# Optimization experiments

Hardware: AMD Instinct MI355X
Metric: run time of the kernel (lower is better)

The kernel has to match this reference:

```python
import jax, jax.numpy as jnp
import numpy as np

NUM_HEADS = 8
DIM = 256
HEAD_DIM = DIM // NUM_HEADS  # 32
CPB_HIDDEN = 512
FFN_HIDDEN = 1024


def _relative_position_cpb(query_size, key_size, pretrain_size):
    # TransNeXt-style continuous position bias table + index (query==key grid here)
    qh, qw = query_size
    kh, kw = key_size
    ph, pw = pretrain_size
    aqh = np.arange(qh, dtype=np.float64)
    akh = np.arange(kh, dtype=np.float64)
    aqw = np.arange(qw, dtype=np.float64)
    akw = np.arange(kw, dtype=np.float64)
    kH, kW = np.meshgrid(akh, akw, indexing='ij')
    qH, qW = np.meshgrid(aqh, aqw, indexing='ij')
    rel_h = (qH.reshape(-1)[:, None] - kH.reshape(-1)[None, :]) / (ph - 1) * 8.0
    rel_w = (qW.reshape(-1)[:, None] - kW.reshape(-1)[None, :]) / (pw - 1) * 8.0
    rel = np.stack([rel_h, rel_w], axis=-1).reshape(-1, 2)
    table, idx = np.unique(rel, return_inverse=True, axis=0)
    table = np.sign(table) * np.log2(np.abs(table) + 1.0) / np.log2(8.0)
    return idx.astype(np.int32).reshape(-1), table.astype(np.float32)


def setup_inputs() -> dict:
    key = jax.random.key(0)
    ks = jax.random.split(key, 16)
    B, C, H, W = 8, 256, 128, 128
    q = jax.random.normal(ks[0], (B, C, H, W), dtype=jnp.float32)
    kv = jax.random.normal(ks[1], (B, C, H, W), dtype=jnp.float32)
    rel_idx_np, rel_table_np = _relative_position_cpb((32, 32), (32, 32), (32, 32))
    s = 0.02
    inp = {
        'q': q,
        'kv': kv,
        'rel_pos_index': jnp.asarray(rel_idx_np),
        'rel_coords_table': jnp.asarray(rel_table_np),
        'Wq': jax.random.normal(ks[2], (DIM, DIM), jnp.float32) * s,
        'bq': jnp.zeros((DIM,), jnp.float32),
        'Wkv': jax.random.normal(ks[3], (DIM, 2 * DIM), jnp.float32) * s,
        'bkv': jnp.zeros((2 * DIM,), jnp.float32),
        'Wo': jax.random.normal(ks[4], (DIM, DIM), jnp.float32) * s,
        'bo': jnp.zeros((DIM,), jnp.float32),
        'cpb_w1': jax.random.normal(ks[5], (2, CPB_HIDDEN), jnp.float32) * s,
        'cpb_b1': jnp.zeros((CPB_HIDDEN,), jnp.float32),
        'cpb_w2': jax.random.normal(ks[6], (CPB_HIDDEN, NUM_HEADS), jnp.float32) * s,
        'cpb_b2': jnp.zeros((NUM_HEADS,), jnp.float32),
        'ffn_w1': jax.random.normal(ks[7], (DIM, FFN_HIDDEN), jnp.float32) * s,
        'ffn_b1': jnp.zeros((FFN_HIDDEN,), jnp.float32),
        'ffn_w2': jax.random.normal(ks[8], (FFN_HIDDEN, DIM), jnp.float32) * s,
        'ffn_b2': jnp.zeros((DIM,), jnp.float32),
        'ln_g': jnp.ones((DIM,), jnp.float32),
        'ln_b': jnp.zeros((DIM,), jnp.float32),
    }
    return inp


def _resize_bilinear(x, size):
    # matches torch F.interpolate(mode='bilinear', align_corners=False)
    return jax.image.resize(x, (x.shape[0], x.shape[1], size[0], size[1]),
                            method='linear', antialias=False)


def _layernorm(x, g, b, eps=1e-5):
    mu = jnp.mean(x, axis=-1, keepdims=True)
    var = jnp.mean(jnp.square(x - mu), axis=-1, keepdims=True)
    return (x - mu) * jax.lax.rsqrt(var + eps) * g + b


def _fpn_forward(q, kv, rel_pos_index, rel_coords_table, Wq, bq, Wkv, bkv, Wo, bo,
                 cpb_w1, cpb_b1, cpb_w2, cpb_b2, ffn_w1, ffn_b1, ffn_w2, ffn_b2, ln_g, ln_b):
    x = q
    B, C, H, W = q.shape
    pH = H // 4
    pW = H // 4  # note: original code uses h for both, matching square inputs
    N = pH * pW

    qd = jax.nn.relu(_resize_bilinear(q, (pH, pW)))   # [B,C,pH,pW] (dropout p=0)
    kvd = jax.nn.relu(_resize_bilinear(kv, (pH, pW)))
    qt = qd.reshape(B, C, N).transpose(0, 2, 1)   # [B,N,C]
    kvt = kvd.reshape(B, C, N).transpose(0, 2, 1)  # [B,N,C]

    # --- BVAM: cross-attention with continuous relative position bias ---
    qh = (qt @ Wq + bq).reshape(B, N, NUM_HEADS, HEAD_DIM).transpose(0, 2, 1, 3)  # [B,h,N,d]
    kvp = (kvt @ Wkv + bkv).reshape(B, N, 2, NUM_HEADS, HEAD_DIM).transpose(2, 0, 3, 1, 4)
    k, v = kvp[0], kvp[1]  # [B,h,N,d]

    cpb = jax.nn.relu(rel_coords_table @ cpb_w1 + cpb_b1) @ cpb_w2 + cpb_b2  # [L,h]
    bias = cpb[rel_pos_index].reshape(N, N, NUM_HEADS).transpose(2, 0, 1)    # [h,N,N]

    scale = 1.0 / jnp.sqrt(jnp.float32(HEAD_DIM))
    logits = jnp.einsum('bhnd,bhmd->bhnm', qh, k) * scale + bias[None]
    attn = jax.nn.softmax(logits, axis=-1)
    out = jnp.einsum('bhnm,bhmd->bhnd', attn, v)
    out = out.transpose(0, 2, 1, 3).reshape(B, N, C) @ Wo + bo  # [B,N,C]

    # --- FFN (post-norm, gelu) ---
    ff = jax.nn.gelu(out @ ffn_w1 + ffn_b1, approximate=False) @ ffn_w2 + ffn_b2
    y = _layernorm(out + ff, ln_g, ln_b)  # [B,N,C]

    # back to spatial, upsample, residual
    y = y.transpose(0, 2, 1).reshape(B, C, pH, pW)
    y = jax.nn.relu(_resize_bilinear(y, (H, W)))
    return x + y


def reference(q, kv, rel_pos_index, rel_coords_table, Wq, bq, Wkv, bkv, Wo, bo,
              cpb_w1, cpb_b1, cpb_w2, cpb_b2, ffn_w1, ffn_b1, ffn_w2, ffn_b2, ln_g, ln_b):
    return _fpn_forward(q, kv, rel_pos_index, rel_coords_table, Wq, bq, Wkv, bkv, Wo, bo,
                        cpb_w1, cpb_b1, cpb_w2, cpb_b2, ffn_w1, ffn_b1, ffn_w2, ffn_b2, ln_g, ln_b)
```

## Files before the change

### kernel.cpp

```cpp
#include <hip/hip_runtime.h>
#include <hip/hip_bf16.h>
#include <hip/hip_fp16.h>

typedef __hip_bfloat16 bf16;
typedef __attribute__((ext_vector_type(8))) __bf16 bf16x8;
typedef __attribute__((ext_vector_type(4))) __bf16 bf16x4;
typedef __attribute__((ext_vector_type(4))) float f32x4;
typedef __attribute__((ext_vector_type(4))) float f4;

__device__ __forceinline__ void gload_lds16(const bf16* g, bf16* l)
{
    __builtin_amdgcn_global_load_lds((const __attribute__((address_space(1))) void*)g,
                                     (__attribute__((address_space(3))) void*)l, 16, 0, 0);
}

__global__ __launch_bounds__(256) void prep_kernel(
    const float* __restrict__ tab, const float* __restrict__ w1, const float* __restrict__ b1,
    const float* __restrict__ w2, const float* __restrict__ b2, float* __restrict__ cpbout, int L, int ncpb,
    const float* __restrict__ Wq, const float* __restrict__ Wkv, const float* __restrict__ Wo,
    const float* __restrict__ fw1, const float* __restrict__ fw2,
    bf16* __restrict__ WqT, bf16* __restrict__ WkvT, bf16* __restrict__ WoT,
    bf16* __restrict__ W1T, bf16* __restrict__ W2T,
    const float* __restrict__ qsrc, const float* __restrict__ kvsrc,
    bf16* __restrict__ qdst, bf16* __restrict__ kvdst)
{
    __shared__ float o[32][33];
    const int t = threadIdx.x;
    int bid = blockIdx.x;
    if (bid < ncpb) {
        int l = bid * 32 + (t >> 3);
        int js = t & 7;
        bool valid = l < L;
        float t0 = valid ? tab[2 * l] : 0.f, t1 = valid ? tab[2 * l + 1] : 0.f;
        float acc[8];
#pragma unroll
        for (int hh = 0; hh < 8; ++hh) acc[hh] = 0.f;
        for (int j = js; j < 512; j += 8) {
            float hv = fmaxf(t0 * w1[j] + t1 * w1[512 + j] + b1[j], 0.f);
            f4 w2a = *(const f4*)&w2[j * 8];
            f4 w2b = *(const f4*)&w2[j * 8 + 4];
#pragma unroll
            for (int hh = 0; hh < 4; ++hh) { acc[hh] += hv * w2a[hh]; acc[4 + hh] += hv * w2b[hh]; }
        }
#pragma unroll
        for (int d = 1; d < 8; d <<= 1)
#pragma unroll
            for (int hh = 0; hh < 8; ++hh) acc[hh] += __shfl_xor(acc[hh], d);
        if (js == 0 && valid)
#pragma unroll
            for (int hh = 0; hh < 8; ++hh) cpbout[(size_t)hh * L + l] = acc[hh] + b2[hh];
        return;
    }
    bid -= ncpb;
    if (bid < 768) {
        const float* W; bf16* WT; int K, N, base;
        if (bid < 64)        { W = Wq;  WT = WqT;  K = 256;  N = 256;  base = 0; }
        else if (bid < 192)  { W = Wkv; WT = WkvT; K = 256;  N = 512;  base = 64; }
        else if (bid < 256)  { W = Wo;  WT = WoT;  K = 256;  N = 256;  base = 192; }
        else if (bid < 512)  { W = fw1; WT = W1T;  K = 256;  N = 1024; base = 256; }
        else                 { W = fw2; WT = W2T;  K = 1024; N = 256;  base = 512; }
        int lid = bid - base;
        int tn = N >> 5;
        int k0 = (lid / tn) << 5, n0 = (lid % tn) << 5;
        {
            int r = t >> 3, cc = (t & 7) * 4;
            *(f4*)&o[r][cc] = *(const f4*)&W[(size_t)(k0 + r) * N + n0 + cc];
        }
        __syncthreads();
        {
            int n = t >> 3, kk = (t & 7) * 4;
            bf16 tmp[4];
#pragma unroll
            for (int i = 0; i < 4; ++i) tmp[i] = (bf16)o[kk + i][n];
            *(bf16x4*)&WT[(size_t)(n0 + n) * K + k0 + kk] = *(const bf16x4*)tmp;
        }
        return;
    }
    bid -= 768;
    {
        const float* src = bid < 2048 ? qsrc : kvsrc;
        bf16* dst = bid < 2048 ? qdst : kvdst;
        int bb2 = bid & 2047;
        int cc = bb2 & 7, i = (bb2 >> 3) & 31, b = bb2 >> 8;
#pragma unroll
        for (int p = 0; p < 4; ++p) {
            int id = p * 256 + t;
            int c = id >> 5, j = id & 31;
            const float* r = src + ((size_t)(b * 256 + cc * 32 + c) * 128 + 4 * i + 1) * 128 + 4 * j;
            float4 r1 = *(const float4*)r;
            float4 r2 = *(const float4*)(r + 128);
            o[c][j] = 0.25f * (r1.y + r1.z + r2.y + r2.z);
        }
        __syncthreads();
        {
            int j = t >> 3, c4 = (t & 7) * 4;
            bf16 tmp[4];
#pragma unroll
            for (int k = 0; k < 4; ++k) tmp[k] = (bf16)fmaxf(o[c4 + k][j], 0.f);
            *(bf16x4*)&dst[(size_t)(b * 1024 + i * 32 + j) * 256 + cc * 32 + c4] = *(const bf16x4*)tmp;
        }
    }
}

template<int BM, int BN>
__device__ __forceinline__ void gemm_core(
    const bf16* __restrict__ A, const bf16* __restrict__ BT, int K,
    int m0, int n0, bf16* As, bf16* Bs, f32x4 (&acc)[BM / 32][BN / 32])
{
    constexpr int MI = BM / 32, NJ = BN / 32;
    const int tid = threadIdx.x;
    const int lane = tid & 63, wid = tid >> 6;
    const int lo = lane & 15, hi = lane >> 4;
    const int wr = wid >> 1, wc = wid & 1;
#pragma unroll
    for (int i = 0; i < MI; ++i)
#pragma unroll
        for (int j = 0; j < NJ; ++j) acc[i][j] = f32x4{0.f, 0.f, 0.f, 0.f};

    for (int k0 = 0; k0 < K; k0 += 64) {
        __syncthreads();
#pragma unroll
        for (int p = 0; p < BM / 32; ++p) {
            int f = p * 256 + wid * 64 + lane;
            int row = f >> 3, cs = f & 7;
            gload_lds16(&A[(size_t)(m0 + row) * K + k0 + ((cs ^ (row & 7)) * 8)],
                        As + (size_t)(p * 256 + wid * 64) * 8);
        }
#pragma unroll
        for (int p = 0; p < BN / 32; ++p) {
            int f = p * 256 + wid * 64 + lane;
            int row = f >> 3, cs = f & 7;
            gload_lds16(&BT[(size_t)(n0 + row) * K + k0 + ((cs ^ (row & 7)) * 8)],
                        Bs + (size_t)(p * 256 + wid * 64) * 8);
        }
        __syncthreads();
        bf16x8 af[2][MI], bfr[2][NJ];
#pragma unroll
        for (int kk = 0; kk < 2; ++kk) {
#pragma unroll
            for (int i = 0; i < MI; ++i) {
                int row = wr * (BM / 2) + i * 16 + lo;
                af[kk][i] = *(const bf16x8*)&As[row * 64 + (((kk * 4 + hi) ^ (lo & 7)) * 8)];
            }
#pragma unroll
            for (int j = 0; j < NJ; ++j) {
                int row = wc * (BN / 2) + j * 16 + lo;
                bfr[kk][j] = *(const bf16x8*)&Bs[row * 64 + (((kk * 4 + hi) ^ (lo & 7)) * 8)];
            }
        }
#pragma unroll
        for (int kk = 0; kk < 2; ++kk)
#pragma unroll
            for (int i = 0; i < MI; ++i)
#pragma unroll
                for (int j = 0; j < NJ; ++j)
                    acc[i][j] = __builtin_amdgcn_mfma_f32_16x16x32_bf16(af[kk][i], bfr[kk][j], acc[i][j], 0, 0, 0);
    }
}

template<int BM, int BN>
__global__ __launch_bounds__(256) void gemm_bt(
    const bf16* __restrict__ A, const bf16* __restrict__ BT,
    const float* __restrict__ bias, bf16* __restrict__ Cb, float* __restrict__ Cf,
    const bf16* __restrict__ resid, int M, int N, int K, int act)
{
    constexpr int MI = BM / 32, NJ = BN / 32;
    __shared__ __align__(16) bf16 As[BM * 64];
    __shared__ __align__(16) bf16 Bs[BN * 64];
    const int tid = threadIdx.x;
    const int lane = tid & 63, wid = tid >> 6;
    const int lo = lane & 15, hi = lane >> 4;
    const int m0 = blockIdx.x * BM, n0 = blockIdx.y * BN;
    const int wr = wid >> 1, wc = wid & 1;
    f32x4 acc[MI][NJ];
    gemm_core<BM, BN>(A, BT, K, m0, n0, As, Bs, acc);
#pragma unroll
    for (int i = 0; i < MI; ++i)
#pragma unroll
        for (int j = 0; j < NJ; ++j) {
            int col = n0 + wc * (BN / 2) + j * 16 + lo;
            float bv = bias[col];
#pragma unroll
            for (int r = 0; r < 4; ++r) {
                int row = m0 + wr * (BM / 2) + i * 16 + hi * 4 + r;
                float v = acc[i][j][r] + bv;
                if (act == 1) v = 0.5f * v * (1.f + erff(v * 0.70710678118654752f));
                if (resid) v += (float)resid[(size_t)row * N + col];
                if (Cb) Cb[(size_t)row * N + col] = (bf16)v;
                else    Cf[(size_t)row * N + col] = v;
            }
        }
}

__global__ __launch_bounds__(256) void gemm_qkv(
    const bf16* __restrict__ qt, const bf16* __restrict__ WqT, const float* __restrict__ bq,
    bf16* __restrict__ qhb,
    const bf16* __restrict__ kvt, const bf16* __restrict__ WkvT, const float* __restrict__ bkv,
    bf16* __restrict__ kvpb, bf16* __restrict__ vT,
    const int* __restrict__ ridx, const float* __restrict__ cpbh,
    bf16* __restrict__ biasF, int L)
{
    __shared__ __align__(16) bf16 As[64 * 64];
    __shared__ __align__(16) bf16 Bs[64 * 64];
    const int tid = threadIdx.x;
    const int lane = tid & 63, wid = tid >> 6;
    const int lo = lane & 15, hi = lane >> 4;
    const int by = blockIdx.y;
    if (by >= 12) {
        __shared__ int rix[32][32];
        int id = (by - 12) * 128 + blockIdx.x;
        int qtb = id >> 5, mt = id & 31;
        {
            int q = tid >> 3, m4 = (tid & 7) * 4;
            *(int4*)&rix[q][m4] = *(const int4*)&ridx[(size_t)(qtb * 32 + q) * 1024 + mt * 32 + m4];
        }
        __syncthreads();
        const int qj = (tid >> 6) & 1, hg = tid >> 7;
        int lidx[8];
#pragma unroll
        for (int j = 0; j < 8; ++j) {
            int kf = j >> 2, r = j & 3;
            lidx[j] = rix[qj * 16 + lo][kf * 16 + hi * 4 + r];
        }
#pragma unroll
        for (int hh = 0; hh < 4; ++hh) {
            int h = hg * 4 + hh;
            const float* ct = cpbh + (size_t)h * L;
            bf16 vals[8];
#pragma unroll
            for (int j = 0; j < 8; ++j) vals[j] = (bf16)ct[lidx[j]];
            size_t off = ((((size_t)(h * 32 + qtb) * 32 + mt) * 2 + qj) * 64 + lane) * 8;
            *(bf16x8*)&biasF[off] = *(const bf16x8*)vals;
        }
        return;
    }
    const int wr = wid >> 1, wc = wid & 1;
    const bf16 *A, *BT; const float* bias; int n0;
    if (by < 4)      { A = qt;  BT = WqT;  bias = bq;  n0 = by * 64; }
    else             { A = kvt; BT = WkvT; bias = bkv; n0 = (by - 4) * 64; }
    const int m0 = blockIdx.x * 64;
    f32x4 acc[2][2];
    gemm_core<64, 64>(A, BT, 256, m0, n0, As, Bs, acc);
#pragma unroll
    for (int i = 0; i < 2; ++i)
#pragma unroll
        for (int j = 0; j < 2; ++j) {
            int col = n0 + wc * 32 + j * 16 + lo;
            float bv = bias[col];
            if (by < 4) {
#pragma unroll
                for (int r = 0; r < 4; ++r) {
                    int row = m0 + wr * 32 + i * 16 + hi * 4 + r;
                    qhb[(size_t)row * 256 + col] = (bf16)(acc[i][j][r] + bv);
                }
            } else if (by < 8) {
#pragma unroll
                for (int r = 0; r < 4; ++r) {
                    int row = m0 + wr * 32 + i * 16 + hi * 4 + r;
                    kvpb[(size_t)row * 512 + col] = (bf16)(acc[i][j][r] + bv);
                }
            } else {
                int vcol = col - 256;
                int h = vcol >> 5, d = vcol & 31;
                int b = m0 >> 10;
                int mbase = (m0 & 1023) + wr * 32 + i * 16 + hi * 4;
                bf16 tmp[4];
#pragma unroll
                for (int r = 0; r < 4; ++r) tmp[r] = (bf16)(acc[i][j][r] + bv);
                *(bf16x4*)&vT[(size_t)((b * 8 + h) * 32 + d) * 1024 + mbase] = *(const bf16x4*)tmp;
            }
        }
}

__global__ __launch_bounds__(256) void ffn2_ln_kernel(
    const bf16* __restrict__ A, const bf16* __restrict__ BT,
    const float* __restrict__ bias, const bf16* __restrict__ resid,
    const float* __restrict__ g, const float* __restrict__ bb,
    bf16* __restrict__ ysp)
{
    __shared__ __align__(16) bf16 As[16 * 64];
    __shared__ __align__(16) bf16 Bs[256 * 64];
    __shared__ float buf[16][260];
    const int tid = threadIdx.x;
    const int lane = tid & 63, wid = tid >> 6;
    const int lo = lane & 15, hi = lane >> 4;
    const int m0 = blockIdx.x * 16;
    f32x4 acc[4];
#pragma unroll
    for (int j = 0; j < 4; ++j) acc[j] = f32x4{0.f, 0.f, 0.f, 0.f};

    for (int k0 = 0; k0 < 1024; k0 += 64) {
        __syncthreads();
        if (tid < 128) {
            int row = tid >> 3, cs = tid & 7;
            gload_lds16(&A[(size_t)(m0 + row) * 1024 + k0 + ((cs ^ (row & 7)) * 8)],
                        As + (size_t)(wid * 64) * 8);
        }
#pragma unroll
        for (int p = 0; p < 8; ++p) {
            int f = p * 256 + tid, row = f >> 3, cs = f & 7;
            gload_lds16(&BT[(size_t)row * 1024 + k0 + ((cs ^ (row & 7)) * 8)],
                        Bs + (size_t)(p * 256 + wid * 64) * 8);
        }
        __syncthreads();
        bf16x8 af[2], bfr[2][4];
#pragma unroll
        for (int kk = 0; kk < 2; ++kk) {
            af[kk] = *(const bf16x8*)&As[lo * 64 + (((kk * 4 + hi) ^ (lo & 7)) * 8)];
#pragma unroll
            for (int j = 0; j < 4; ++j) {
                int row = wid * 64 + j * 16 + lo;
                bfr[kk][j] = *(const bf16x8*)&Bs[row * 64 + (((kk * 4 + hi) ^ (lo & 7)) * 8)];
            }
        }
#pragma unroll
        for (int kk = 0; kk < 2; ++kk)
#pragma unroll
            for (int j = 0; j < 4; ++j)
                acc[j] = __builtin_amdgcn_mfma_f32_16x16x32_bf16(af[kk], bfr[kk][j], acc[j], 0, 0, 0);
    }
#pragma unroll
    for (int j = 0; j < 4; ++j) {
        int col = wid * 64 + j * 16 + lo;
        float bv = bias[col];
#pragma unroll
        for (int r = 0; r < 4; ++r) {
            int lr = hi * 4 + r;
            buf[lr][col] = acc[j][r] + bv + (float)resid[(size_t)(m0 + lr) * 256 + col];
        }
    }
    __syncthreads();
#pragma unroll
    for (int rr = 0; rr < 4; ++rr) {
        int row = wid * 4 + rr;
        f4 x = *(const f4*)&buf[row][lane * 4];
        float s = x[0] + x[1] + x[2] + x[3];
#pragma unroll
        for (int d = 1; d < 64; d <<= 1) s += __shfl_xor(s, d);
        float mean = s * (1.f / 256.f);
        f4 dv = {x[0] - mean, x[1] - mean, x[2] - mean, x[3] - mean};
        float s2 = dv[0] * dv[0] + dv[1] * dv[1] + dv[2] * dv[2] + dv[3] * dv[3];
#pragma unroll
        for (int d = 1; d < 64; d <<= 1) s2 += __shfl_xor(s2, d);
        float rstd = rsqrtf(s2 * (1.f / 256.f) + 1e-5f);
        f4 o = {dv[0] * rstd, dv[1] * rstd, dv[2] * rstd, dv[3] * rstd};
        *(f4*)&buf[row][lane * 4] = o;
    }
    __syncthreads();
    float gc = g[tid], bc = bb[tid];
    int b = m0 >> 10, n0l = m0 & 1023;
    bf16* dst = &ysp[((size_t)(b * 256 + tid) << 10) + n0l];
#pragma unroll
    for (int p = 0; p < 2; ++p) {
        bf16 tmp[8];
#pragma unroll
        for (int k = 0; k < 8; ++k) tmp[k] = (bf16)(buf[p * 8 + k][tid] * gc + bc);
        *(bf16x8*)&dst[p * 8] = *(const bf16x8*)tmp;
    }
}

__global__ __launch_bounds__(256) void attn_kernel(
    const bf16* __restrict__ qh, const bf16* __restrict__ kvp, const bf16* __restrict__ vT,
    const bf16* __restrict__ biasF, bf16* __restrict__ attnout)
{
    __shared__ __align__(16) bf16 Ps[4][32 * 40];
    __shared__ __align__(16) __half accs[4][32][34];
    __shared__ float pm[4][32], pl[4][32];
    const int tid = threadIdx.x, lane = tid & 63, wid = tid >> 6;
    const int lo = lane & 15, hi = lane >> 4;
    const int qt = blockIdx.x, n0 = qt * 32;
    const int h = blockIdx.y;
    const int b = blockIdx.z;
    const float scale = 0.17677669529663687f;
    const f32x4 zero4 = {0.f, 0.f, 0.f, 0.f};

    bf16x8 qf[2];
#pragma unroll
    for (int qj = 0; qj < 2; ++qj)
        qf[qj] = *(const bf16x8*)&qh[(size_t)(b * 1024 + n0 + qj * 16 + lo) * 256 + h * 32 + hi * 8];

    f32x4 acc[2][2];
#pragma unroll
    for (int i = 0; i < 2; ++i)
#pragma unroll
        for (int j = 0; j < 2; ++j) acc[i][j] = zero4;
    float mrow[2] = {-1e30f, -1e30f}, lrow[2] = {0.f, 0.f};

    bf16* Pw = Ps[wid];

    for (int t = wid; t < 32; t += 4) {
        const int m0 = t * 32;
        bf16x8 kfr0 = *(const bf16x8*)&kvp[(size_t)(b * 1024 + m0 + lo) * 512 + h * 32 + hi * 8];
        bf16x8 kfr1 = *(const bf16x8*)&kvp[(size_t)(b * 1024 + m0 + 16 + lo) * 512 + h * 32 + hi * 8];
        bf16x8 va0 = *(const bf16x8*)&vT[(size_t)((b * 8 + h) * 32 + lo) * 1024 + m0 + hi * 8];
        bf16x8 va1 = *(const bf16x8*)&vT[(size_t)((b * 8 + h) * 32 + 16 + lo) * 1024 + m0 + hi * 8];
        size_t boff = (((size_t)(h * 32 + qt) * 32 + t) * 2 * 64 + lane) * 8;
        bf16x8 bv0 = *(const bf16x8*)&biasF[boff];
        bf16x8 bv1 = *(const bf16x8*)&biasF[boff + 512];

        f32x4 s[2][2];
        s[0][0] = __builtin_amdgcn_mfma_f32_16x16x32_bf16(kfr0, qf[0], zero4, 0, 0, 0);
        s[0][1] = __builtin_amdgcn_mfma_f32_16x16x32_bf16(kfr0, qf[1], zero4, 0, 0, 0);
        s[1][0] = __builtin_amdgcn_mfma_f32_16x16x32_bf16(kfr1, qf[0], zero4, 0, 0, 0);
        s[1][1] = __builtin_amdgcn_mfma_f32_16x16x32_bf16(kfr1, qf[1], zero4, 0, 0, 0);
#pragma unroll
        for (int kf = 0; kf < 2; ++kf)
#pragma unroll
            for (int r = 0; r < 4; ++r) {
                s[kf][0][r] = s[kf][0][r] * scale + (float)bv0[kf * 4 + r];
                s[kf][1][r] = s[kf][1][r] * scale + (float)bv1[kf * 4 + r];
            }
#pragma unroll
        for (int qj = 0; qj < 2; ++qj) {
            float mx = fmaxf(fmaxf(fmaxf(s[0][qj][0], s[0][qj][1]), fmaxf(s[0][qj][2], s[0][qj][3])),
                             fmaxf(fmaxf(s[1][qj][0], s[1][qj][1]), fmaxf(s[1][qj][2], s[1][qj][3])));
            mx = fmaxf(mx, __shfl_xor(mx, 16));
            mx = fmaxf(mx, __shfl_xor(mx, 32));
            float mnew = fmaxf(mrow[qj], mx);
            float alpha = __expf(mrow[qj] - mnew);
            float rs = 0.f;
#pragma unroll
            for (int kf = 0; kf < 2; ++kf)
#pragma unroll
                for (int r = 0; r < 4; ++r) {
                    float p = __expf(s[kf][qj][r] - mnew);
                    s[kf][qj][r] = p;
                    rs += p;
                }
            rs += __shfl_xor(rs, 16);
            rs += __shfl_xor(rs, 32);
            lrow[qj] = lrow[qj] * alpha + rs;
            mrow[qj] = mnew;
#pragma unroll
            for (int di = 0; di < 2; ++di)
#pragma unroll
                for (int r = 0; r < 4; ++r) acc[di][qj][r] *= alpha;
        }
#pragma unroll
        for (int qj = 0; qj < 2; ++qj)
#pragma unroll
            for (int kf = 0; kf < 2; ++kf)
#pragma unroll
                for (int r = 0; r < 4; ++r)
                    Pw[(qj * 16 + lo) * 40 + kf * 16 + hi * 4 + r] = (bf16)s[kf][qj][r];
        bf16x8 pb0 = *(const bf16x8*)&Pw[lo * 40 + hi * 8];
        bf16x8 pb1 = *(const bf16x8*)&Pw[(16 + lo) * 40 + hi * 8];
        acc[0][0] = __builtin_amdgcn_mfma_f32_16x16x32_bf16(va0, pb0, acc[0][0], 0, 0, 0);
        acc[0][1] = __builtin_amdgcn_mfma_f32_16x16x32_bf16(va0, pb1, acc[0][1], 0, 0, 0);
        acc[1][0] = __builtin_amdgcn_mfma_f32_16x16x32_bf16(va1, pb0, acc[1][0], 0, 0, 0);
        acc[1][1] = __builtin_amdgcn_mfma_f32_16x16x32_bf16(va1, pb1, acc[1][1], 0, 0, 0);
    }
#pragma unroll
    for (int di = 0; di < 2; ++di)
#pragma unroll
        for (int qj = 0; qj < 2; ++qj)
#pragma unroll
            for (int r = 0; r < 4; ++r)
                accs[wid][di * 16 + hi * 4 + r][qj * 16 + lo] = __float2half(acc[di][qj][r]);
    if (hi == 0) {
#pragma unroll
        for (int qj = 0; qj < 2; ++qj) {
            pm[wid][qj * 16 + lo] = mrow[qj];
            pl[wid][qj * 16 + lo] = lrow[qj];
        }
    }
    __syncthreads();
    int q = tid >> 3, d0 = (tid & 7) * 4;
    float M = fmaxf(fmaxf(pm[0][q], pm[1][q]), fmaxf(pm[2][q], pm[3][q]));
    float f0 = __expf(pm[0][q] - M), f1 = __expf(pm[1][q] - M);
    float f2 = __expf(pm[2][q] - M), f3 = __expf(pm[3][q] - M);
    float inv = 1.f / (pl[0][q] * f0 + pl[1][q] * f1 + pl[2][q] * f2 + pl[3][q] * f3);
    bf16 tmp[4];
#pragma unroll
    for (int j = 0; j < 4; ++j) {
        int d = d0 + j;
        float o = f0 * (float)accs[0][d][q] + f1 * (float)accs[1][d][q] +
                  f2 * (float)accs[2][d][q] + f3 * (float)accs[3][d][q];
        tmp[j] = (bf16)(o * inv);
    }
    *(bf16x4*)&attnout[(size_t)(b * 1024 + n0 + q) * 256 + h * 32 + d0] = *(const bf16x4*)tmp;
}

__global__ __launch_bounds__(256) void upsample_kernel(const float* __restrict__ x,
    const bf16* __restrict__ ysp, float* __restrict__ out)
{
    int idx = blockIdx.x * 256 + threadIdx.x;
    int w4 = idx & 31; int r1 = idx >> 5;
    int hh = r1 & 127; int r2 = r1 >> 7;
    int c = r2 & 255; int b = r2 >> 8;
    float chh = 0.25f * hh - 0.375f;
    float fi = floorf(chh);
    float fh = chh - fi;
    int i0 = (int)fi;
    int ia = i0 < 0 ? 0 : i0;
    int ib = (i0 + 1) > 31 ? 31 : (i0 + 1);
    const bf16* yr = ysp + ((size_t)(b * 256 + c) << 10);
    const bf16* ra = yr + ia * 32;
    const bf16* rb = yr + ib * 32;
    f4 xv = *(const f4*)&x[(size_t)idx * 4];
    f4 o;
#pragma unroll
    for (int k = 0; k < 4; ++k) {
        int ww = w4 * 4 + k;
        float cww = 0.25f * ww - 0.375f;
        float fj = floorf(cww);
        float fw = cww - fj;
        int j0 = (int)fj;
        int ja = j0 < 0 ? 0 : j0;
        int jb = (j0 + 1) > 31 ? 31 : (j0 + 1);
        float v = (1.f - fh) * ((1.f - fw) * (float)ra[ja] + fw * (float)ra[jb]) +
                  fh * ((1.f - fw) * (float)rb[ja] + fw * (float)rb[jb]);
        o[k] = xv[k] + fmaxf(v, 0.f);
    }
    *(f4*)&out[(size_t)idx * 4] = o;
}

extern "C" void kernel_launch(void* const* d_in, const int* in_sizes, int n_in,
                              void* d_out, int out_size, void* d_ws, size_t ws_size,
                              hipStream_t stream)
{
    (void)n_in; (void)out_size; (void)ws_size;
    const float* q    = (const float*)d_in[0];
    const float* kv   = (const float*)d_in[1];
    const int*   ridx = (const int*)d_in[2];
    const float* rtab = (const float*)d_in[3];
    const float* Wq   = (const float*)d_in[4];
    const float* bq   = (const float*)d_in[5];
    const float* Wkv  = (const float*)d_in[6];
    const float* bkv  = (const float*)d_in[7];
    const float* Wo   = (const float*)d_in[8];
    const float* bo   = (const float*)d_in[9];
    const float* cw1  = (const float*)d_in[10];
    const float* cb1  = (const float*)d_in[11];
    const float* cw2  = (const float*)d_in[12];
    const float* cb2  = (const float*)d_in[13];
    const float* fw1  = (const float*)d_in[14];
    const float* fb1  = (const float*)d_in[15];
    const float* fw2  = (const float*)d_in[16];
    const float* fb2  = (const float*)d_in[17];
    const float* lng  = (const float*)d_in[18];
    const float* lnb  = (const float*)d_in[19];
    const int L = in_sizes[3] / 2;
    const int ncpb = (L + 31) / 32;

    char* w = (char*)d_ws;
    auto alloc = [&](size_t bytes) { char* p = w; w += (bytes + 255) & ~(size_t)255; return p; };
    bf16* qt      = (bf16*)alloc(8192ull * 256 * 2);
    bf16* kvt     = (bf16*)alloc(8192ull * 256 * 2);
    bf16* qhb     = (bf16*)alloc(8192ull * 256 * 2);
    bf16* kvpb    = (bf16*)alloc(8192ull * 512 * 2);
    bf16* vTb     = (bf16*)alloc(8ull * 8 * 32 * 1024 * 2);
    bf16* attnb   = (bf16*)alloc(8192ull * 256 * 2);
    bf16* outb    = (bf16*)alloc(8192ull * 256 * 2);
    bf16* ffh     = (bf16*)alloc(8192ull * 1024 * 2);
    bf16* ysp     = (bf16*)alloc(8ull * 256 * 1024 * 2);
    bf16* WqT     = (bf16*)alloc(256ull * 256 * 2);
    bf16* WkvT    = (bf16*)alloc(512ull * 256 * 2);
    bf16* WoT     = (bf16*)alloc(256ull * 256 * 2);
    bf16* W1T     = (bf16*)alloc(1024ull * 256 * 2);
    bf16* W2T     = (bf16*)alloc(256ull * 1024 * 2);
    float* cpbb   = (float*)alloc((size_t)8 * L * 4);
    bf16* biasF   = ffh;

    prep_kernel<<<dim3(ncpb + 768 + 4096), 256, 0, stream>>>(
        rtab, cw1, cb1, cw2, cb2, cpbb, L, ncpb,
        Wq, Wkv, Wo, fw1, fw2, WqT, WkvT, WoT, W1T, W2T,
        q, kv, qt, kvt);
    gemm_qkv<<<dim3(128, 20), 256, 0, stream>>>(qt, WqT, bq, qhb, kvt, WkvT, bkv, kvpb, vTb,
                                                ridx, cpbb, biasF, L);
    attn_kernel<<<dim3(32, 8, 8), 256, 0, stream>>>(qhb, kvpb, vTb, biasF, attnb);
    gemm_bt<64, 64><<<dim3(128, 4), 256, 0, stream>>>(attnb, WoT, bo, outb, nullptr, nullptr, 8192, 256, 256, 0);
    gemm_bt<128, 64><<<dim3(64, 16), 256, 0, stream>>>(outb, W1T, fb1, ffh, nullptr, nullptr, 8192, 1024, 256, 1);
    ffn2_ln_kernel<<<dim3(512), 256, 0, stream>>>(ffh, W2T, fb2, outb, lng, lnb, ysp);
    upsample_kernel<<<dim3(32768), 256, 0, stream>>>(q, ysp, (float*)d_out);
}
```

Baseline: 189.2 us.

## Fuse QKV, attention, out-proj and FFN into persistent kernel with grid barriers

Replaces five separate kernel launches (QKV GEMM plus bias gather, attention, output projection, FFN1, FFN2 with layernorm) with a single persistent 512-block kernel. The kernel loops over virtual block ids per phase and uses an atomic generation-counter grid barrier between phases. Shared memory is a single char buffer reinterpreted per phase. This removes launch overhead and inter-kernel drain gaps. In exchange it relies on all blocks being co-resident without a cooperative launch, adds barrier spin cost, and fixes the block count at 2 per CU.

```diff
diff --git a/kernel.cpp b/kernel.cpp
--- a/kernel.cpp
+++ b/kernel.cpp
@@ -8,10 +8,33 @@
 typedef __attribute__((ext_vector_type(4))) float f32x4;
 typedef __attribute__((ext_vector_type(4))) float f4;
 
+#define NBLK 512
+
 __device__ __forceinline__ void gload_lds16(const bf16* g, bf16* l)
 {
     __builtin_amdgcn_global_load_lds((const __attribute__((address_space(1))) void*)g,
                                      (__attribute__((address_space(3))) void*)l, 16, 0, 0);
+}
+
+__device__ __forceinline__ void grid_sync(int* bar)
+{
+    __syncthreads();
+    if (threadIdx.x == 0) {
+        int* cnt = bar;
+        int* gen = bar + 1;
+        int g = __hip_atomic_load(gen, __ATOMIC_ACQUIRE, __HIP_MEMORY_SCOPE_AGENT);
+        __threadfence();
+        int t = __hip_atomic_fetch_add(cnt, 1, __ATOMIC_ACQ_REL, __HIP_MEMORY_SCOPE_AGENT);
+        if (t == NBLK - 1) {
+            __hip_atomic_store(cnt, 0, __ATOMIC_RELEASE, __HIP_MEMORY_SCOPE_AGENT);
+            __hip_atomic_fetch_add(gen, 1, __ATOMIC_ACQ_REL, __HIP_MEMORY_SCOPE_AGENT);
+        } else {
+            while (__hip_atomic_load(gen, __ATOMIC_ACQUIRE, __HIP_MEMORY_SCOPE_AGENT) == g)
+                __builtin_amdgcn_s_sleep(2);
+        }
+        __threadfence();
+    }
+    __syncthreads();
 }
 
 __global__ __launch_bounds__(256) void prep_kernel(
@@ -156,63 +179,26 @@
                 for (int j = 0; j < NJ; ++j)
                     acc[i][j] = __builtin_amdgcn_mfma_f32_16x16x32_bf16(af[kk][i], bfr[kk][j], acc[i][j], 0, 0, 0);
     }
-}
-
-template<int BM, int BN>
-__global__ __launch_bounds__(256) void gemm_bt(
-    const bf16* __restrict__ A, const bf16* __restrict__ BT,
-    const float* __restrict__ bias, bf16* __restrict__ Cb, float* __restrict__ Cf,
-    const bf16* __restrict__ resid, int M, int N, int K, int act)
-{
-    constexpr int MI = BM / 32, NJ = BN / 32;
-    __shared__ __align__(16) bf16 As[BM * 64];
-    __shared__ __align__(16) bf16 Bs[BN * 64];
+    __syncthreads();
+}
+
+__device__ void phase_qkv(char* smem, int vb,
+    const bf16* qt, const bf16* WqT, const float* bq, bf16* qhb,
+    const bf16* kvt, const bf16* WkvT, const float* bkv, bf16* kvpb, bf16* vT,
+    const int* ridx, const float* cpbh, bf16* biasF, int L)
+{
     const int tid = threadIdx.x;
     const int lane = tid & 63, wid = tid >> 6;
     const int lo = lane & 15, hi = lane >> 4;
-    const int m0 = blockIdx.x * BM, n0 = blockIdx.y * BN;
-    const int wr = wid >> 1, wc = wid & 1;
-    f32x4 acc[MI][NJ];
-    gemm_core<BM, BN>(A, BT, K, m0, n0, As, Bs, acc);
-#pragma unroll
-    for (int i = 0; i < MI; ++i)
-#pragma unroll
-        for (int j = 0; j < NJ; ++j) {
-            int col = n0 + wc * (BN / 2) + j * 16 + lo;
-            float bv = bias[col];
-#pragma unroll
-            for (int r = 0; r < 4; ++r) {
-                int row = m0 + wr * (BM / 2) + i * 16 + hi * 4 + r;
-                float v = acc[i][j][r] + bv;
-                if (act == 1) v = 0.5f * v * (1.f + erff(v * 0.70710678118654752f));
-                if (resid) v += (float)resid[(size_t)row * N + col];
-                if (Cb) Cb[(size_t)row * N + col] = (bf16)v;
-                else    Cf[(size_t)row * N + col] = v;
-            }
-        }
-}
-
-__global__ __launch_bounds__(256) void gemm_qkv(
-    const bf16* __restrict__ qt, const bf16* __restrict__ WqT, const float* __restrict__ bq,
-    bf16* __restrict__ qhb,
-    const bf16* __restrict__ kvt, const bf16* __restrict__ WkvT, const float* __restrict__ bkv,
-    bf16* __restrict__ kvpb, bf16* __restrict__ vT,
-    const int* __restrict__ ridx, const float* __restrict__ cpbh,
-    bf16* __restrict__ biasF, int L)
-{
-    __shared__ __align__(16) bf16 As[64 * 64];
-    __shared__ __align__(16) bf16 Bs[64 * 64];
-    const int tid = threadIdx.x;
-    const int lane = tid & 63, wid = tid >> 6;
-    const int lo = lane & 15, hi = lane >> 4;
-    const int by = blockIdx.y;
+    const int bx = vb & 127, by = vb >> 7;
     if (by >= 12) {
-        __shared__ int rix[32][32];
-        int id = (by - 12) * 128 + blockIdx.x;
+        __syncthreads();
+        int* rix = (int*)smem;
+        int id = (by - 12) * 128 + bx;
         int qtb = id >> 5, mt = id & 31;
         {
             int q = tid >> 3, m4 = (tid & 7) * 4;
-            *(int4*)&rix[q][m4] = *(const int4*)&ridx[(size_t)(qtb * 32 + q) * 1024 + mt * 32 + m4];
+            *(int4*)&rix[q * 32 + m4] = *(const int4*)&ridx[(size_t)(qtb * 32 + q) * 1024 + mt * 32 + m4];
         }
         __syncthreads();
         const int qj = (tid >> 6) & 1, hg = tid >> 7;
@@ -220,7 +206,7 @@
 #pragma unroll
         for (int j = 0; j < 8; ++j) {
             int kf = j >> 2, r = j & 3;
-            lidx[j] = rix[qj * 16 + lo][kf * 16 + hi * 4 + r];
+            lidx[j] = rix[(qj * 16 + lo) * 32 + kf * 16 + hi * 4 + r];
         }
 #pragma unroll
         for (int hh = 0; hh < 4; ++hh) {
@@ -232,13 +218,16 @@
             size_t off = ((((size_t)(h * 32 + qtb) * 32 + mt) * 2 + qj) * 64 + lane) * 8;
             *(bf16x8*)&biasF[off] = *(const bf16x8*)vals;
         }
+        __syncthreads();
         return;
     }
+    bf16* As = (bf16*)smem;
+    bf16* Bs = (bf16*)(smem + 8192);
     const int wr = wid >> 1, wc = wid & 1;
     const bf16 *A, *BT; const float* bias; int n0;
     if (by < 4)      { A = qt;  BT = WqT;  bias = bq;  n0 = by * 64; }
     else             { A = kvt; BT = WkvT; bias = bkv; n0 = (by - 4) * 64; }
-    const int m0 = blockIdx.x * 64;
+    const int m0 = bx * 64;
     f32x4 acc[2][2];
     gemm_core<64, 64>(A, BT, 256, m0, n0, As, Bs, acc);
 #pragma unroll
@@ -272,105 +261,19 @@
         }
 }
 
-__global__ __launch_bounds__(256) void ffn2_ln_kernel(
-    const bf16* __restrict__ A, const bf16* __restrict__ BT,
-    const float* __restrict__ bias, const bf16* __restrict__ resid,
-    const float* __restrict__ g, const float* __restrict__ bb,
-    bf16* __restrict__ ysp)
-{
-    __shared__ __align__(16) bf16 As[16 * 64];
-    __shared__ __align__(16) bf16 Bs[256 * 64];
-    __shared__ float buf[16][260];
-    const int tid = threadIdx.x;
-    const int lane = tid & 63, wid = tid >> 6;
-    const int lo = lane & 15, hi = lane >> 4;
-    const int m0 = blockIdx.x * 16;
-    f32x4 acc[4];
-#pragma unroll
-    for (int j = 0; j < 4; ++j) acc[j] = f32x4{0.f, 0.f, 0.f, 0.f};
-
-    for (int k0 = 0; k0 < 1024; k0 += 64) {
-        __syncthreads();
-        if (tid < 128) {
-            int row = tid >> 3, cs = tid & 7;
-            gload_lds16(&A[(size_t)(m0 + row) * 1024 + k0 + ((cs ^ (row & 7)) * 8)],
-                        As + (size_t)(wid * 64) * 8);
-        }
-#pragma unroll
-        for (int p = 0; p < 8; ++p) {
-            int f = p * 256 + tid, row = f >> 3, cs = f & 7;
-            gload_lds16(&BT[(size_t)row * 1024 + k0 + ((cs ^ (row & 7)) * 8)],
-                        Bs + (size_t)(p * 256 + wid * 64) * 8);
-        }
-        __syncthreads();
-        bf16x8 af[2], bfr[2][4];
-#pragma unroll
-        for (int kk = 0; kk < 2; ++kk) {
-            af[kk] = *(const bf16x8*)&As[lo * 64 + (((kk * 4 + hi) ^ (lo & 7)) * 8)];
-#pragma unroll
-            for (int j = 0; j < 4; ++j) {
-                int row = wid * 64 + j * 16 + lo;
-                bfr[kk][j] = *(const bf16x8*)&Bs[row * 64 + (((kk * 4 + hi) ^ (lo & 7)) * 8)];
-            }
-        }
-#pragma unroll
-        for (int kk = 0; kk < 2; ++kk)
-#pragma unroll
-            for (int j = 0; j < 4; ++j)
-                acc[j] = __builtin_amdgcn_mfma_f32_16x16x32_bf16(af[kk], bfr[kk][j], acc[j], 0, 0, 0);
-    }
-#pragma unroll
-    for (int j = 0; j < 4; ++j) {
-        int col = wid * 64 + j * 16 + lo;
-        float bv = bias[col];
-#pragma unroll
-        for (int r = 0; r < 4; ++r) {
-            int lr = hi * 4 + r;
-            buf[lr][col] = acc[j][r] + bv + (float)resid[(size_t)(m0 + lr) * 256 + col];
-        }
-    }
-    __syncthreads();
-#pragma unroll
-    for (int rr = 0; rr < 4; ++rr) {
-        int row = wid * 4 + rr;
-        f4 x = *(const f4*)&buf[row][lane * 4];
-        float s = x[0] + x[1] + x[2] + x[3];
-#pragma unroll
-        for (int d = 1; d < 64; d <<= 1) s += __shfl_xor(s, d);
-        float mean = s * (1.f / 256.f);
-        f4 dv = {x[0] - mean, x[1] - mean, x[2] - mean, x[3] - mean};
-        float s2 = dv[0] * dv[0] + dv[1] * dv[1] + dv[2] * dv[2] + dv[3] * dv[3];
-#pragma unroll
-        for (int d = 1; d < 64; d <<= 1) s2 += __shfl_xor(s2, d);
-        float rstd = rsqrtf(s2 * (1.f / 256.f) + 1e-5f);
-        f4 o = {dv[0] * rstd, dv[1] * rstd, dv[2] * rstd, dv[3] * rstd};
-        *(f4*)&buf[row][lane * 4] = o;
-    }
-    __syncthreads();
-    float gc = g[tid], bc = bb[tid];
-    int b = m0 >> 10, n0l = m0 & 1023;
-    bf16* dst = &ysp[((size_t)(b * 256 + tid) << 10) + n0l];
-#pragma unroll
-    for (int p = 0; p < 2; ++p) {
-        bf16 tmp[8];
-#pragma unroll
-        for (int k = 0; k < 8; ++k) tmp[k] = (bf16)(buf[p * 8 + k][tid] * gc + bc);
-        *(bf16x8*)&dst[p * 8] = *(const bf16x8*)tmp;
-    }
-}
-
-__global__ __launch_bounds__(256) void attn_kernel(
-    const bf16* __restrict__ qh, const bf16* __restrict__ kvp, const bf16* __restrict__ vT,
-    const bf16* __restrict__ biasF, bf16* __restrict__ attnout)
-{
-    __shared__ __align__(16) bf16 Ps[4][32 * 40];
-    __shared__ __align__(16) __half accs[4][32][34];
-    __shared__ float pm[4][32], pl[4][32];
+__device__ void phase_attn(char* smem, int vb,
+    const bf16* qh, const bf16* kvp, const bf16* vT,
+    const bf16* biasF, bf16* attnout)
+{
+    bf16* Ps = (bf16*)smem;
+    __half* accs = (__half*)(smem + 10240);
+    float* pm = (float*)(smem + 18944);
+    float* pl = (float*)(smem + 19456);
     const int tid = threadIdx.x, lane = tid & 63, wid = tid >> 6;
     const int lo = lane & 15, hi = lane >> 4;
-    const int qt = blockIdx.x, n0 = qt * 32;
-    const int h = blockIdx.y;
-    const int b = blockIdx.z;
+    const int qt = vb & 31, n0 = qt * 32;
+    const int h = (vb >> 5) & 7;
+    const int b = vb >> 8;
     const float scale = 0.17677669529663687f;
     const f32x4 zero4 = {0.f, 0.f, 0.f, 0.f};
 
@@ -386,7 +289,7 @@
         for (int j = 0; j < 2; ++j) acc[i][j] = zero4;
     float mrow[2] = {-1e30f, -1e30f}, lrow[2] = {0.f, 0.f};
 
-    bf16* Pw = Ps[wid];
+    bf16* Pw = Ps + wid * (32 * 40);
 
     for (int t = wid; t < 32; t += 4) {
         const int m0 = t * 32;
@@ -456,29 +359,173 @@
         for (int qj = 0; qj < 2; ++qj)
 #pragma unroll
             for (int r = 0; r < 4; ++r)
-                accs[wid][di * 16 + hi * 4 + r][qj * 16 + lo] = __float2half(acc[di][qj][r]);
+                accs[((wid * 32) + di * 16 + hi * 4 + r) * 34 + qj * 16 + lo] = __float2half(acc[di][qj][r]);
     if (hi == 0) {
 #pragma unroll
         for (int qj = 0; qj < 2; ++qj) {
-            pm[wid][qj * 16 + lo] = mrow[qj];
-            pl[wid][qj * 16 + lo] = lrow[qj];
+            pm[wid * 32 + qj * 16 + lo] = mrow[qj];
+            pl[wid * 32 + qj * 16 + lo] = lrow[qj];
         }
     }
     __syncthreads();
     int q = tid >> 3, d0 = (tid & 7) * 4;
-    float M = fmaxf(fmaxf(pm[0][q], pm[1][q]), fmaxf(pm[2][q], pm[3][q]));
-    float f0 = __expf(pm[0][q] - M), f1 = __expf(pm[1][q] - M);
-    float f2 = __expf(pm[2][q] - M), f3 = __expf(pm[3][q] - M);
-    float inv = 1.f / (pl[0][q] * f0 + pl[1][q] * f1 + pl[2][q] * f2 + pl[3][q] * f3);
+    float M = fmaxf(fmaxf(pm[q], pm[32 + q]), fmaxf(pm[64 + q], pm[96 + q]));
+    float f0 = __expf(pm[q] - M), f1 = __expf(pm[32 + q] - M);
+    float f2 = __expf(pm[64 + q] - M), f3 = __expf(pm[96 + q] - M);
+    float inv = 1.f / (pl[q] * f0 + pl[32 + q] * f1 + pl[64 + q] * f2 + pl[96 + q] * f3);
     bf16 tmp[4];
 #pragma unroll
     for (int j = 0; j < 4; ++j) {
         int d = d0 + j;
-        float o = f0 * (float)accs[0][d][q] + f1 * (float)accs[1][d][q] +
-                  f2 * (float)accs[2][d][q] + f3 * (float)accs[3][d][q];
+        float o = f0 * (float)accs[(0 * 32 + d) * 34 + q] + f1 * (float)accs[(1 * 32 + d) * 34 + q] +
+                  f2 * (float)accs[(2 * 32 + d) * 34 + q] + f3 * (float)accs[(3 * 32 + d) * 34 + q];
         tmp[j] = (bf16)(o * inv);
     }
     *(bf16x4*)&attnout[(size_t)(b * 1024 + n0 + q) * 256 + h * 32 + d0] = *(const bf16x4*)tmp;
+    __syncthreads();
+}
+
+template<int BM, int BN>
+__device__ void phase_gemm(char* smem, int bx, int by,
+    const bf16* A, const bf16* BT, const float* bias, bf16* Cb, int N, int K, int act)
+{
+    bf16* As = (bf16*)smem;
+    bf16* Bs = (bf16*)(smem + BM * 64 * 2);
+    constexpr int MI = BM / 32, NJ = BN / 32;
+    const int tid = threadIdx.x;
+    const int lane = tid & 63, wid = tid >> 6;
+    const int lo = lane & 15, hi = lane >> 4;
+    const int m0 = bx * BM, n0 = by * BN;
+    const int wr = wid >> 1, wc = wid & 1;
+    f32x4 acc[MI][NJ];
+    gemm_core<BM, BN>(A, BT, K, m0, n0, As, Bs, acc);
+#pragma unroll
+    for (int i = 0; i < MI; ++i)
+#pragma unroll
+        for (int j = 0; j < NJ; ++j) {
+            int col = n0 + wc * (BN / 2) + j * 16 + lo;
+            float bv = bias[col];
+#pragma unroll
+            for (int r = 0; r < 4; ++r) {
+                int row = m0 + wr * (BM / 2) + i * 16 + hi * 4 + r;
+                float v = acc[i][j][r] + bv;
+                if (act == 1) v = 0.5f * v * (1.f + erff(v * 0.70710678118654752f));
+                Cb[(size_t)row * N + col] = (bf16)v;
+            }
+        }
+}
+
+__device__ void phase_ffn2ln(char* smem, int vb,
+    const bf16* A, const bf16* BT, const float* bias, const bf16* resid,
+    const float* g, const float* bb, bf16* ysp)
+{
+    bf16* As = (bf16*)smem;
+    bf16* Bs = (bf16*)(smem + 2048);
+    float (*buf)[260] = (float(*)[260])(smem + 34816);
+    const int tid = threadIdx.x;
+    const int lane = tid & 63, wid = tid >> 6;
+    const int lo = lane & 15, hi = lane >> 4;
+    const int m0 = vb * 16;
+    f32x4 acc[4];
+#pragma unroll
+    for (int j = 0; j < 4; ++j) acc[j] = f32x4{0.f, 0.f, 0.f, 0.f};
+
+    for (int k0 = 0; k0 < 1024; k0 += 64) {
+        __syncthreads();
+        if (tid < 128) {
+            int row = tid >> 3, cs = tid & 7;
+            gload_lds16(&A[(size_t)(m0 + row) * 1024 + k0 + ((cs ^ (row & 7)) * 8)],
+                        As + (size_t)(wid * 64) * 8);
+        }
+#pragma unroll
+        for (int p = 0; p < 8; ++p) {
+            int f = p * 256 + tid, row = f >> 3, cs = f & 7;
+            gload_lds16(&BT[(size_t)row * 1024 + k0 + ((cs ^ (row & 7)) * 8)],
+                        Bs + (size_t)(p * 256 + wid * 64) * 8);
+        }
+        __syncthreads();
+        bf16x8 af[2], bfr[2][4];
+#pragma unroll
+        for (int kk = 0; kk < 2; ++kk) {
+            af[kk] = *(const bf16x8*)&As[lo * 64 + (((kk * 4 + hi) ^ (lo & 7)) * 8)];
+#pragma unroll
+            for (int j = 0; j < 4; ++j) {
+                int row = wid * 64 + j * 16 + lo;
+                bfr[kk][j] = *(const bf16x8*)&Bs[row * 64 + (((kk * 4 + hi) ^ (lo & 7)) * 8)];
+            }
+        }
+#pragma unroll
+        for (int kk = 0; kk < 2; ++kk)
+#pragma unroll
+            for (int j = 0; j < 4; ++j)
+                acc[j] = __builtin_amdgcn_mfma_f32_16x16x32_bf16(af[kk], bfr[kk][j], acc[j], 0, 0, 0);
+    }
+#pragma unroll
+    for (int j = 0; j < 4; ++j) {
+        int col = wid * 64 + j * 16 + lo;
+        float bv = bias[col];
+#pragma unroll
+        for (int r = 0; r < 4; ++r) {
+            int lr = hi * 4 + r;
+            buf[lr][col] = acc[j][r] + bv + (float)resid[(size_t)(m0 + lr) * 256 + col];
+        }
+    }
+    __syncthreads();
+#pragma unroll
+    for (int rr = 0; rr < 4; ++rr) {
+        int row = wid * 4 + rr;
+        f4 x = *(const f4*)&buf[row][lane * 4];
+        float s = x[0] + x[1] + x[2] + x[3];
+#pragma unroll
+        for (int d = 1; d < 64; d <<= 1) s += __shfl_xor(s, d);
+        float mean = s * (1.f / 256.f);
+        f4 dv = {x[0] - mean, x[1] - mean, x[2] - mean, x[3] - mean};
+        float s2 = dv[0] * dv[0] + dv[1] * dv[1] + dv[2] * dv[2] + dv[3] * dv[3];
+#pragma unroll
+        for (int d = 1; d < 64; d <<= 1) s2 += __shfl_xor(s2, d);
+        float rstd = rsqrtf(s2 * (1.f / 256.f) + 1e-5f);
+        f4 o = {dv[0] * rstd, dv[1] * rstd, dv[2] * rstd, dv[3] * rstd};
+        *(f4*)&buf[row][lane * 4] = o;
+    }
+    __syncthreads();
+    float gc = g[tid], bc = bb[tid];
+    int b = m0 >> 10, n0l = m0 & 1023;
+    bf16* dst = &ysp[((size_t)(b * 256 + tid) << 10) + n0l];
+#pragma unroll
+    for (int p = 0; p < 2; ++p) {
+        bf16 tmp[8];
+#pragma unroll
+        for (int k = 0; k < 8; ++k) tmp[k] = (bf16)(buf[p * 8 + k][tid] * gc + bc);
+        *(bf16x8*)&dst[p * 8] = *(const bf16x8*)tmp;
+    }
+}
+
+__global__ __launch_bounds__(256, 2) void mid_kernel(
+    const bf16* __restrict__ qt, const bf16* __restrict__ WqT, const float* __restrict__ bq,
+    bf16* __restrict__ qhb,
+    const bf16* __restrict__ kvt, const bf16* __restrict__ WkvT, const float* __restrict__ bkv,
+    bf16* __restrict__ kvpb, bf16* __restrict__ vT,
+    const int* __restrict__ ridx, const float* __restrict__ cpbh, bf16* __restrict__ biasF, int L,
+    bf16* __restrict__ attnb,
+    const bf16* __restrict__ WoT, const float* __restrict__ bo, bf16* __restrict__ outb,
+    const bf16* __restrict__ W1T, const float* __restrict__ fb1, bf16* __restrict__ ffh,
+    const bf16* __restrict__ W2T, const float* __restrict__ fb2,
+    const float* __restrict__ lng, const float* __restrict__ lnb, bf16* __restrict__ ysp,
+    int* __restrict__ bar)
+{
+    __shared__ __align__(16) char smem[51456];
+    for (int vb = blockIdx.x; vb < 2560; vb += NBLK)
+        phase_qkv(smem, vb, qt, WqT, bq, qhb, kvt, WkvT, bkv, kvpb, vT, ridx, cpbh, biasF, L);
+    grid_sync(bar);
+    for (int vb = blockIdx.x; vb < 2048; vb += NBLK)
+        phase_attn(smem, vb, qhb, kvpb, vT, biasF, attnb);
+    grid_sync(bar);
+    phase_gemm<64, 64>(smem, blockIdx.x & 127, blockIdx.x >> 7, attnb, WoT, bo, outb, 256, 256, 0);
+    grid_sync(bar);
+    for (int vb = blockIdx.x; vb < 1024; vb += NBLK)
+        phase_gemm<128, 64>(smem, vb & 63, vb >> 6, outb, W1T, fb1, ffh, 1024, 256, 1);
+    grid_sync(bar);
+    phase_ffn2ln(smem, blockIdx.x, ffh, W2T, fb2, outb, lng, lnb, ysp);
 }
 
 __global__ __launch_bounds__(256) void upsample_kernel(const float* __restrict__ x,
@@ -560,17 +607,17 @@
     bf16* W1T     = (bf16*)alloc(1024ull * 256 * 2);
     bf16* W2T     = (bf16*)alloc(256ull * 1024 * 2);
     float* cpbb   = (float*)alloc((size_t)8 * L * 4);
+    int*  bar     = (int*)alloc(256);
     bf16* biasF   = ffh;
 
+    hipMemsetAsync(bar, 0, 8, stream);
     prep_kernel<<<dim3(ncpb + 768 + 4096), 256, 0, stream>>>(
         rtab, cw1, cb1, cw2, cb2, cpbb, L, ncpb,
         Wq, Wkv, Wo, fw1, fw2, WqT, WkvT, WoT, W1T, W2T,
         q, kv, qt, kvt);
-    gemm_qkv<<<dim3(128, 20), 256, 0, stream>>>(qt, WqT, bq, qhb, kvt, WkvT, bkv, kvpb, vTb,
-                                                ridx, cpbb, biasF, L);
-    attn_kernel<<<dim3(32, 8, 8), 256, 0, stream>>>(qhb, kvpb, vTb, biasF, attnb);
-    gemm_bt<64, 64><<<dim3(128, 4), 256, 0, stream>>>(attnb, WoT, bo, outb, nullptr, nullptr, 8192, 256, 256, 0);
-    gemm_bt<128, 64><<<dim3(64, 16), 256, 0, stream>>>(outb, W1T, fb1, ffh, nullptr, nullptr, 8192, 1024, 256, 1);
-    ffn2_ln_kernel<<<dim3(512), 256, 0, stream>>>(ffh, W2T, fb2, outb, lng, lnb, ysp);
+    mid_kernel<<<dim3(NBLK), 256, 0, stream>>>(
+        qt, WqT, bq, qhb, kvt, WkvT, bkv, kvpb, vTb,
+        ridx, cpbb, biasF, L, attnb,
+        WoT, bo, outb, W1T, fb1, ffh, W2T, fb2, lng, lnb, ysp, bar);
     upsample_kernel<<<dim3(32768), 256, 0, stream>>>(q, ysp, (float*)d_out);
 }
```

New measurement: 473.3 us. 2.5x slower.
